# Kernel tuning notes

Measured on AMD Instinct MI355X. Metric: run time of the kernel, lower is better.

The kernel has to match this reference:

```python
import jax, jax.numpy as jnp
import numpy as np

N = 100000
E = 1600000
F_IN, F_HID, F_OUT = 512, 512, 256
NEG_SLOPE = 0.01  # nn.LeakyReLU default


def setup_inputs() -> dict:
    key = jax.random.key(0)
    ks = jax.random.split(key, 16)
    def lin(k, fi, fo):
        s = 1.0 / np.sqrt(fi)
        return jax.random.uniform(k, (fi, fo), jnp.float32, -s, s)
    inp = {
        'x': jax.random.normal(ks[0], (N, F_IN), jnp.float32),
        'edge_index': jax.random.randint(ks[1], (2, E), 0, N, jnp.int64),
        'W1': lin(ks[2], F_IN, F_HID), 'b1': jnp.zeros((F_HID,), jnp.float32),
        'W2': lin(ks[3], F_HID, F_HID), 'b2': jnp.zeros((F_HID,), jnp.float32),
        'W3': lin(ks[4], F_HID, F_HID), 'b3': jnp.zeros((F_HID,), jnp.float32),
        'W4': lin(ks[5], F_HID, F_OUT), 'b4': jnp.zeros((F_OUT,), jnp.float32),
        'fcW1': lin(ks[6], F_OUT, 64), 'fcb1': jnp.zeros((64,), jnp.float32),
        'fcW2': lin(ks[7], 64, 1), 'fcb2': jnp.zeros((1,), jnp.float32),
    }
    return inp


def _gcn_norm(edge_index):
    # PyG gcn_norm with add_self_loops=True: deg counts incoming edges + 1 self loop
    src, dst = edge_index[0], edge_index[1]
    deg = jax.ops.segment_sum(jnp.ones((E,), jnp.float32), dst, num_segments=N) + 1.0
    dis = jax.lax.rsqrt(deg)  # deg >= 1 always (self loops)
    edge_norm = dis[src] * dis[dst]  # [E]
    self_norm = dis * dis            # [N], norm for the added self loop
    return src, dst, edge_norm, self_norm


def _gcn_layer(x, src, dst, edge_norm, self_norm, W, b):
    xw = x @ W  # transform-then-propagate (in < out not an issue here)
    agg = jax.ops.segment_sum(xw[src] * edge_norm[:, None], dst, num_segments=N)
    return agg + self_norm[:, None] * xw + b


def leaky(x):
    return jnp.where(x >= 0, x, NEG_SLOPE * x)


def reference(x, edge_index, W1, b1, W2, b2, W3, b3, W4, b4, fcW1, fcb1, fcW2, fcb2):
    src, dst, en, sn = _gcn_norm(edge_index)
    h = leaky(_gcn_layer(x, src, dst, en, sn, W1, b1))
    h = leaky(_gcn_layer(h, src, dst, en, sn, W2, b2))
    h = leaky(_gcn_layer(h, src, dst, en, sn, W3, b3))
    h = leaky(_gcn_layer(h, src, dst, en, sn, W4, b4))
    g = jnp.mean(h, axis=0, keepdims=True)  # global_mean_pool, batch=None -> [1, F_OUT]
    g = leaky(g @ fcW1 + fcb1)
    # dropout is identity in eval mode
    g = g @ fcW2 + fcb2
    return jax.nn.sigmoid(g)  # [1, 1]
```

## Files before the change

kernel.cpp:

```cpp
#include <hip/hip_runtime.h>
#include <hip/hip_bf16.h>
#include <cstdint>
#include <cstddef>


typedef unsigned short u16;
typedef unsigned char u8;
typedef unsigned int u32;
typedef u16 u16x4 __attribute__((ext_vector_type(4)));
typedef u16 u16x8 __attribute__((ext_vector_type(8)));
typedef u32 u32x2 __attribute__((ext_vector_type(2)));
typedef float f32x2 __attribute__((ext_vector_type(2)));
typedef float f32x4 __attribute__((ext_vector_type(4)));

__device__ __forceinline__ u16 f2bf(float f) {
  u32 u = __builtin_bit_cast(u32, f);
  u += 0x7fffu + ((u >> 16) & 1u);
  return (u16)(u >> 16);
}
__device__ __forceinline__ float bf2f(u16 h) {
  return __builtin_bit_cast(float, (u32)h << 16);
}
__device__ __forceinline__ void g2lds16(const void* g, void* l) {
  __builtin_amdgcn_global_load_lds((__attribute__((address_space(1))) void*)g,
                                   (__attribute__((address_space(3))) void*)l, 16, 0, 0);
}

__global__ __launch_bounds__(256) void init_kernel(int* __restrict__ deg,
                                                   int* __restrict__ cursor,
                                                   float* __restrict__ pool, int N) {
  int i = blockIdx.x * 256 + threadIdx.x;
  if (i < N) { deg[i] = 0; cursor[i] = 0; }
  if (i < 256) pool[i] = 0.f;
}

__global__ void detect_kernel(const int* __restrict__ ei, int* __restrict__ flag) {
  __shared__ int nz;
  if (threadIdx.x == 0) nz = 0;
  __syncthreads();
  if (ei[2 * threadIdx.x + 1] != 0) atomicAdd(&nz, 1);
  __syncthreads();
  if (threadIdx.x == 0) *flag = (nz == 0) ? 1 : 0;
}

__device__ __forceinline__ int ld_src(const int* ei, int E, int e, int f64) {
  return f64 ? (int)((const long long*)ei)[e] : ei[e];
}
__device__ __forceinline__ int ld_dst(const int* ei, int E, int e, int f64) {
  return f64 ? (int)((const long long*)ei)[(long long)E + e] : ei[E + e];
}

__global__ __launch_bounds__(256) void degree_kernel(const int* __restrict__ ei,
                                                     const int* __restrict__ flag,
                                                     int* __restrict__ deg, int E) {
  int e = blockIdx.x * 256 + threadIdx.x;
  if (e >= E) return;
  int f = *flag;
  atomicAdd(&deg[ld_dst(ei, E, e, f)], 1);
}

__global__ __launch_bounds__(256) void dis_kernel(const int* __restrict__ deg,
                                                  float* __restrict__ dis, int N) {
  int i = blockIdx.x * 256 + threadIdx.x;
  if (i < N) dis[i] = rsqrtf((float)deg[i] + 1.0f);
}

__global__ __launch_bounds__(1024) void scan1_kernel(const int* __restrict__ deg,
                                                     int* __restrict__ rs,
                                                     int* __restrict__ bsum, int N) {
  __shared__ int s[1024];
  int tid = threadIdx.x;
  int i = blockIdx.x * 1024 + tid;
  int v = (i < N) ? deg[i] : 0;
  s[tid] = v;
  __syncthreads();
  for (int off = 1; off < 1024; off <<= 1) {
    int t = (tid >= off) ? s[tid - off] : 0;
    __syncthreads();
    s[tid] += t;
    __syncthreads();
  }
  if (i < N) rs[i] = s[tid] - v;
  if (tid == 1023) bsum[blockIdx.x] = s[1023];
}

__global__ __launch_bounds__(1024) void scan2_kernel(const int* __restrict__ bsum,
                                                     int* __restrict__ boff, int nb) {
  __shared__ int s[1024];
  int tid = threadIdx.x;
  int v = (tid < nb) ? bsum[tid] : 0;
  s[tid] = v;
  __syncthreads();
  for (int off = 1; off < 1024; off <<= 1) {
    int t = (tid >= off) ? s[tid - off] : 0;
    __syncthreads();
    s[tid] += t;
    __syncthreads();
  }
  if (tid < nb) boff[tid] = s[tid] - v;
}

__global__ __launch_bounds__(256) void scan3_kernel(int* __restrict__ rs,
                                                    const int* __restrict__ boff, int N) {
  int i = blockIdx.x * 256 + threadIdx.x;
  if (i < N) rs[i] += boff[i >> 10];
}

__global__ __launch_bounds__(256) void fill_kernel(const int* __restrict__ ei,
                                                   const int* __restrict__ flag,
                                                   const int* __restrict__ rs,
                                                   int* __restrict__ cursor,
                                                   int* __restrict__ colv, int E) {
  int e = blockIdx.x * 256 + threadIdx.x;
  if (e >= E) return;
  int f = *flag;
  int s = ld_src(ei, E, e, f);
  int d = ld_dst(ei, E, e, f);
  int p = atomicAdd(&cursor[d], 1);
  colv[rs[d] + p] = s;
}

__global__ __launch_bounds__(256) void convx_kernel(const float* __restrict__ x,
                                                    u8* __restrict__ x8, size_t n) {
  size_t i = ((size_t)blockIdx.x * 256 + threadIdx.x) * 4;
  if (i >= n) return;
  float4 v = *reinterpret_cast<const float4*>(x + i);
  int lo = __builtin_amdgcn_cvt_pk_fp8_f32(v.x, v.y, 0, false);
  int r = __builtin_amdgcn_cvt_pk_fp8_f32(v.z, v.w, lo, true);
  size_t row = i >> 9;
  int col = (int)(i & 511);
  int sw = ((int)(row & 7)) << 3;
  *reinterpret_cast<u32*>(x8 + row * 512 + (col ^ sw)) = (u32)r;
}

__global__ __launch_bounds__(256) void convw_kernel(const float* __restrict__ W,
                                                    u8* __restrict__ Wt, int Nout) {
  int id = blockIdx.x * 256 + threadIdx.x;
  if (id >= 512 * Nout) return;
  int k = id / Nout, nn = id - k * Nout;
  float v = W[id];
  int e = __builtin_amdgcn_cvt_pk_fp8_f32(v, v, 0, false);
  Wt[nn * 512 + (k ^ ((nn & 7) << 3))] = (u8)e;
}

__global__ __launch_bounds__(256, 2)
void gemm8_kernel(const u8* __restrict__ A, const u8* __restrict__ Bt,
                  u8* __restrict__ Cout, int M, int Nout) {
  __shared__ u8 sA[128 * 64];
  __shared__ u8 sB[128 * 64];
  const int tid = threadIdx.x;
  const int wave = tid >> 6, lane = tid & 63;
  const int m0 = blockIdx.x * 128;
  const int n0 = blockIdx.y * 128;
  const int wm = (wave >> 1) * 64, wn = (wave & 1) * 64;
  const int srow = tid >> 2;
  const int soff = (tid & 3) * 16;
  const int fr = lane & 15, fq8 = (lane >> 4) * 8;
  const int xa = (fr & 7) << 3;

  f32x4 acc[4][4];
#pragma unroll
  for (int i = 0; i < 4; ++i)
#pragma unroll
    for (int j = 0; j < 4; ++j) acc[i][j] = (f32x4){0.f, 0.f, 0.f, 0.f};

  int ar0 = m0 + srow;      if (ar0 >= M) ar0 = M - 1;
  int ar1 = m0 + 64 + srow; if (ar1 >= M) ar1 = M - 1;
  const size_t a0 = (size_t)ar0 * 512 + soff;
  const size_t a1 = (size_t)ar1 * 512 + soff;
  const size_t b0 = (size_t)(n0 + srow) * 512 + soff;
  const size_t b1 = (size_t)(n0 + 64 + srow) * 512 + soff;

  for (int k0 = 0; k0 < 512; k0 += 64) {
    g2lds16(A + a0 + k0, &sA[wave * 1024]);
    g2lds16(A + a1 + k0, &sA[4096 + wave * 1024]);
    g2lds16(Bt + b0 + k0, &sB[wave * 1024]);
    g2lds16(Bt + b1 + k0, &sB[4096 + wave * 1024]);
    __builtin_amdgcn_s_waitcnt(0);
    __syncthreads();

    long long af[2][4], bf[2][4];
#pragma unroll
    for (int t = 0; t < 4; ++t) {
      const int ra = (wm + t * 16 + fr) * 64;
      const int rb = (wn + t * 16 + fr) * 64;
#pragma unroll
      for (int s = 0; s < 2; ++s) {
        af[s][t] = *reinterpret_cast<const long long*>(&sA[ra + ((s * 32 + fq8) ^ xa)]);
        bf[s][t] = *reinterpret_cast<const long long*>(&sB[rb + ((s * 32 + fq8) ^ xa)]);
      }
    }
#pragma unroll
    for (int i = 0; i < 4; ++i)
#pragma unroll
      for (int j = 0; j < 4; ++j) {
        acc[i][j] = __builtin_amdgcn_mfma_f32_16x16x32_fp8_fp8(af[0][i], bf[0][j], acc[i][j], 0, 0, 0);
        acc[i][j] = __builtin_amdgcn_mfma_f32_16x16x32_fp8_fp8(af[1][i], bf[1][j], acc[i][j], 0, 0, 0);
      }
    __syncthreads();
  }

  const int crow0 = m0 + wm + ((lane >> 4) << 2);
  const int ccol0 = n0 + wn + (lane & 15);
#pragma unroll
  for (int j = 0; j < 4; ++j) {
    const int col = ccol0 + j * 16;
#pragma unroll
    for (int i = 0; i < 4; ++i)
#pragma unroll
      for (int r = 0; r < 4; ++r) {
        int row = crow0 + i * 16 + r;
        if (row < M) {
          float v = acc[i][j][r];
          int e = __builtin_amdgcn_cvt_pk_fp8_f32(v, v, 0, false);
          Cout[(size_t)row * Nout + (col ^ ((row & 7) << 3))] = (u8)e;
        }
      }
  }
}

__global__ __launch_bounds__(256)
void agg_kernel(const u8* __restrict__ xw, const int* __restrict__ colv,
                const int* __restrict__ rs, const int* __restrict__ deg,
                const float* __restrict__ dis, const float* __restrict__ bias,
                u8* __restrict__ hout, int N) {
  const int wave = threadIdx.x >> 6;
  const int lane = threadIdx.x & 63;
  const int node = blockIdx.x * 4 + wave;
  if (node >= N) return;
  const int start = rs[node];
  const int d = deg[node];
  const float dd = dis[node];
  const int fo = lane * 8;

  f32x2 acc[4];
#pragma unroll
  for (int i = 0; i < 4; ++i) acc[i] = (f32x2){0.f, 0.f};

  const int total = d + 1;
  for (int base = 0; base < total; base += 64) {
    int t = base + lane;
    int s = node;
    float w = 0.f;
    if (t < d)       { s = colv[start + t]; w = dd * dis[s]; }
    else if (t == d) { w = dd * dd; }
    int cnt = total - base;
    if (cnt > 64) cnt = 64;
    int cnt8 = (cnt + 7) & ~7;
    int wi = __builtin_bit_cast(int, w);
    for (int j = 0; j < cnt8; j += 8) {
      u32x2 v[8];
      float ws[8];
#pragma unroll
      for (int k = 0; k < 8; ++k) {
        int sk = __builtin_amdgcn_readlane(s, j + k);
        ws[k] = __builtin_bit_cast(float, __builtin_amdgcn_readlane(wi, j + k));
        v[k] = *reinterpret_cast<const u32x2*>(xw + (size_t)sk * 512 + (fo ^ ((sk & 7) << 3)));
      }
#pragma unroll
      for (int k = 0; k < 8; ++k) {
        f32x2 p0 = __builtin_amdgcn_cvt_pk_f32_fp8((int)v[k].x, false);
        f32x2 p1 = __builtin_amdgcn_cvt_pk_f32_fp8((int)v[k].x, true);
        f32x2 p2 = __builtin_amdgcn_cvt_pk_f32_fp8((int)v[k].y, false);
        f32x2 p3 = __builtin_amdgcn_cvt_pk_f32_fp8((int)v[k].y, true);
        f32x2 wv = (f32x2){ws[k], ws[k]};
        acc[0] += wv * p0;
        acc[1] += wv * p1;
        acc[2] += wv * p2;
        acc[3] += wv * p3;
      }
    }
  }

  float h[8];
#pragma unroll
  for (int i = 0; i < 8; ++i) {
    float v = (i & 1) ? acc[i >> 1].y : acc[i >> 1].x;
    v += bias[fo + i];
    v = v >= 0.f ? v : 0.01f * v;
    h[i] = v;
  }
  int lo = __builtin_amdgcn_cvt_pk_fp8_f32(h[0], h[1], 0, false);
  lo = __builtin_amdgcn_cvt_pk_fp8_f32(h[2], h[3], lo, true);
  int hi = __builtin_amdgcn_cvt_pk_fp8_f32(h[4], h[5], 0, false);
  hi = __builtin_amdgcn_cvt_pk_fp8_f32(h[6], h[7], hi, true);
  u32x2 o; o.x = (u32)lo; o.y = (u32)hi;
  __builtin_nontemporal_store(o, reinterpret_cast<u32x2*>(
      hout + (size_t)node * 512 + (fo ^ ((node & 7) << 3))));
}

__global__ __launch_bounds__(256)
void agg256_kernel(const u8* __restrict__ xw, const int* __restrict__ colv,
                   const int* __restrict__ rs, const int* __restrict__ deg,
                   const float* __restrict__ dis, const float* __restrict__ bias,
                   u16* __restrict__ hout, int N) {
  const int wave = threadIdx.x >> 6;
  const int lane = threadIdx.x & 63;
  const int node = blockIdx.x * 4 + wave;
  if (node >= N) return;
  const int start = rs[node];
  const int d = deg[node];
  const float dd = dis[node];
  const int fo = lane * 4;

  f32x2 acc[2];
  acc[0] = (f32x2){0.f, 0.f};
  acc[1] = (f32x2){0.f, 0.f};

  const int total = d + 1;
  for (int base = 0; base < total; base += 64) {
    int t = base + lane;
    int s = node;
    float w = 0.f;
    if (t < d)       { s = colv[start + t]; w = dd * dis[s]; }
    else if (t == d) { w = dd * dd; }
    int cnt = total - base;
    if (cnt > 64) cnt = 64;
    int cnt8 = (cnt + 7) & ~7;
    int wi = __builtin_bit_cast(int, w);
    for (int j = 0; j < cnt8; j += 8) {
      u32 v[8];
      float ws[8];
#pragma unroll
      for (int k = 0; k < 8; ++k) {
        int sk = __builtin_amdgcn_readlane(s, j + k);
        ws[k] = __builtin_bit_cast(float, __builtin_amdgcn_readlane(wi, j + k));
        v[k] = *reinterpret_cast<const u32*>(xw + (size_t)sk * 256 + (fo ^ ((sk & 7) << 3)));
      }
#pragma unroll
      for (int k = 0; k < 8; ++k) {
        f32x2 p0 = __builtin_amdgcn_cvt_pk_f32_fp8((int)v[k], false);
        f32x2 p1 = __builtin_amdgcn_cvt_pk_f32_fp8((int)v[k], true);
        f32x2 wv = (f32x2){ws[k], ws[k]};
        acc[0] += wv * p0;
        acc[1] += wv * p1;
      }
    }
  }

  u16x4 o;
#pragma unroll
  for (int i = 0; i < 4; ++i) {
    float v = (i & 1) ? acc[i >> 1].y : acc[i >> 1].x;
    v += bias[fo + i];
    v = v >= 0.f ? v : 0.01f * v;
    o[i] = f2bf(v);
  }
  *reinterpret_cast<u16x4*>(hout + (size_t)node * 256 + fo) = o;
}

__global__ __launch_bounds__(256) void pool_kernel(const u16* __restrict__ h,
                                                   float* __restrict__ pool, int N) {
  __shared__ float lds[8 * 256];
  const int tid = threadIdx.x;
  const int fg = tid & 31;
  const int rg = tid >> 5;
  float acc[8];
#pragma unroll
  for (int i = 0; i < 8; ++i) acc[i] = 0.f;
  for (int r = blockIdx.x * 8 + rg; r < N; r += gridDim.x * 8) {
    u16x8 v = *reinterpret_cast<const u16x8*>(h + (size_t)r * 256 + fg * 8);
#pragma unroll
    for (int i = 0; i < 8; ++i) acc[i] += bf2f(v[i]);
  }
#pragma unroll
  for (int i = 0; i < 8; ++i) lds[rg * 256 + fg * 8 + i] = acc[i];
  __syncthreads();
  float s = 0.f;
#pragma unroll
  for (int g = 0; g < 8; ++g) s += lds[g * 256 + tid];
  atomicAdd(&pool[tid], s);
}

__global__ void fc_kernel(const float* __restrict__ pool, const float* __restrict__ fcW1,
                          const float* __restrict__ fcb1, const float* __restrict__ fcW2,
                          const float* __restrict__ fcb2, float* __restrict__ out,
                          float invN) {
  int j = threadIdx.x;
  float acc = 0.f;
  for (int f = 0; f < 256; ++f) acc += pool[f] * invN * fcW1[f * 64 + j];
  float h = acc + fcb1[j];
  h = h >= 0.f ? h : 0.01f * h;
  float p = h * fcW2[j];
  for (int o = 32; o; o >>= 1) p += __shfl_down(p, o);
  if (j == 0) out[0] = 1.f / (1.f + expf(-(p + fcb2[0])));
}

extern "C" void kernel_launch(void* const* d_in, const int* in_sizes, int n_in,
                              void* d_out, int out_size, void* d_ws, size_t ws_size,
                              hipStream_t stream) {
  const float* x    = (const float*)d_in[0];
  const int*   ei   = (const int*)d_in[1];
  const float* W1   = (const float*)d_in[2];
  const float* b1   = (const float*)d_in[3];
  const float* W2   = (const float*)d_in[4];
  const float* b2   = (const float*)d_in[5];
  const float* W3   = (const float*)d_in[6];
  const float* b3   = (const float*)d_in[7];
  const float* W4   = (const float*)d_in[8];
  const float* b4   = (const float*)d_in[9];
  const float* fcW1 = (const float*)d_in[10];
  const float* fcb1 = (const float*)d_in[11];
  const float* fcW2 = (const float*)d_in[12];
  const float* fcb2 = (const float*)d_in[13];
  float* out = (float*)d_out;

  const int N = in_sizes[0] / 512;
  const int E = in_sizes[1] / 2;

  char* p = (char*)d_ws;
  auto carve = [&](size_t bytes) {
    char* r = p;
    p += (bytes + 255) & ~(size_t)255;
    return r;
  };
  u8*  bufX = (u8*)carve((size_t)N * 512);
  u8*  bufP = (u8*)carve((size_t)N * 512);
  u8*  bufQ = (u8*)carve((size_t)N * 512);
  u16* bufH4 = (u16*)carve((size_t)N * 256 * 2);
  u8* Wt1 = (u8*)carve(512 * 512);
  u8* Wt2 = (u8*)carve(512 * 512);
  u8* Wt3 = (u8*)carve(512 * 512);
  u8* Wt4 = (u8*)carve(512 * 256);
  int* deg    = (int*)carve((size_t)N * 4);
  int* cursor = (int*)carve((size_t)N * 4);
  int* rs     = (int*)carve((size_t)(N + 1) * 4);
  int* colv   = (int*)carve((size_t)E * 4);
  int* bsum   = (int*)carve(1024 * 4);
  int* boff   = (int*)carve(1024 * 4);
  int* flag   = (int*)carve(256);
  float* disv = (float*)carve((size_t)N * 4);
  float* pool = (float*)carve(256 * 4);
  if ((size_t)(p - (char*)d_ws) > ws_size) return;

  const int nb1024 = (N + 1023) / 1024;

  init_kernel<<<(N + 255) / 256, 256, 0, stream>>>(deg, cursor, pool, N);
  detect_kernel<<<1, 256, 0, stream>>>(ei, flag);
  degree_kernel<<<(E + 255) / 256, 256, 0, stream>>>(ei, flag, deg, E);
  dis_kernel<<<(N + 255) / 256, 256, 0, stream>>>(deg, disv, N);
  scan1_kernel<<<nb1024, 1024, 0, stream>>>(deg, rs, bsum, N);
  scan2_kernel<<<1, 1024, 0, stream>>>(bsum, boff, nb1024);
  scan3_kernel<<<(N + 255) / 256, 256, 0, stream>>>(rs, boff, N);
  fill_kernel<<<(E + 255) / 256, 256, 0, stream>>>(ei, flag, rs, cursor, colv, E);

  convx_kernel<<<((size_t)N * 512 / 4 + 255) / 256, 256, 0, stream>>>(x, bufX, (size_t)N * 512);
  convw_kernel<<<(512 * 512 + 255) / 256, 256, 0, stream>>>(W1, Wt1, 512);
  convw_kernel<<<(512 * 512 + 255) / 256, 256, 0, stream>>>(W2, Wt2, 512);
  convw_kernel<<<(512 * 512 + 255) / 256, 256, 0, stream>>>(W3, Wt3, 512);
  convw_kernel<<<(512 * 256 + 255) / 256, 256, 0, stream>>>(W4, Wt4, 256);

  const unsigned gm = (unsigned)((N + 127) / 128);
  const unsigned ga = (unsigned)((N + 3) / 4);

  gemm8_kernel<<<dim3(gm, 4), 256, 0, stream>>>(bufX, Wt1, bufP, N, 512);
  agg_kernel<<<ga, 256, 0, stream>>>(bufP, colv, rs, deg, disv, b1, bufQ, N);
  gemm8_kernel<<<dim3(gm, 4), 256, 0, stream>>>(bufQ, Wt2, bufP, N, 512);
  agg_kernel<<<ga, 256, 0, stream>>>(bufP, colv, rs, deg, disv, b2, bufX, N);
  gemm8_kernel<<<dim3(gm, 4), 256, 0, stream>>>(bufX, Wt3, bufP, N, 512);
  agg_kernel<<<ga, 256, 0, stream>>>(bufP, colv, rs, deg, disv, b3, bufQ, N);
  gemm8_kernel<<<dim3(gm, 2), 256, 0, stream>>>(bufQ, Wt4, bufP, N, 256);
  agg256_kernel<<<ga, 256, 0, stream>>>(bufP, colv, rs, deg, disv, b4, bufH4, N);

  pool_kernel<<<256, 256, 0, stream>>>(bufH4, pool, N);
  fc_kernel<<<1, 64, 0, stream>>>(pool, fcW1, fcb1, fcW2, fcb2, out, 1.0f / (float)N);
}
```

Measured before the change: 1.137 ms.

## Precompute edge weights in CSR, widen gather loads, and remap GEMM blocks per XCD

The CSR fill now stores each edge's source together with its normalization weight, so the aggregation kernels no longer do a dependent dis[s] gather. Aggregation lanes are split into two halves that each handle a different edge and load 16 (or 8) contiguous bytes, with the halves combined by a cross-half shuffle at the end. The GEMM output swizzle is dropped so gathers read contiguous rows, and the GEMM grid is flattened with a block-index remap that keeps M-tiles sharing an A tile on the same XCD. The costs are a doubled edge-array footprint and an extra shuffle reduction per node.

```diff
diff --git a/kernel.cpp b/kernel.cpp
--- a/kernel.cpp
+++ b/kernel.cpp
@@ -10,6 +10,7 @@
 typedef u16 u16x4 __attribute__((ext_vector_type(4)));
 typedef u16 u16x8 __attribute__((ext_vector_type(8)));
 typedef u32 u32x2 __attribute__((ext_vector_type(2)));
+typedef u32 u32x4 __attribute__((ext_vector_type(4)));
 typedef float f32x2 __attribute__((ext_vector_type(2)));
 typedef float f32x4 __attribute__((ext_vector_type(4)));
 
@@ -110,14 +111,19 @@
                                                    const int* __restrict__ flag,
                                                    const int* __restrict__ rs,
                                                    int* __restrict__ cursor,
-                                                   int* __restrict__ colv, int E) {
+                                                   const float* __restrict__ dis,
+                                                   u32x2* __restrict__ ev, int E) {
   int e = blockIdx.x * 256 + threadIdx.x;
   if (e >= E) return;
   int f = *flag;
   int s = ld_src(ei, E, e, f);
   int d = ld_dst(ei, E, e, f);
   int p = atomicAdd(&cursor[d], 1);
-  colv[rs[d] + p] = s;
+  float w = dis[s] * dis[d];
+  u32x2 t;
+  t.x = (u32)s;
+  t.y = __builtin_bit_cast(u32, w);
+  ev[rs[d] + p] = t;
 }
 
 __global__ __launch_bounds__(256) void convx_kernel(const float* __restrict__ x,
@@ -145,13 +151,19 @@
 
 __global__ __launch_bounds__(256, 2)
 void gemm8_kernel(const u8* __restrict__ A, const u8* __restrict__ Bt,
-                  u8* __restrict__ Cout, int M, int Nout) {
+                  u8* __restrict__ Cout, int M, int Nout, int gm, int lgy) {
+  const int id = blockIdx.x;
+  const int xcd = id & 7, q = id >> 3;
+  const int by = q & ((1 << lgy) - 1);
+  const int bx = ((q >> lgy) << 3) + xcd;
+  if (bx >= gm) return;
+
   __shared__ u8 sA[128 * 64];
   __shared__ u8 sB[128 * 64];
   const int tid = threadIdx.x;
   const int wave = tid >> 6, lane = tid & 63;
-  const int m0 = blockIdx.x * 128;
-  const int n0 = blockIdx.y * 128;
+  const int m0 = bx * 128;
+  const int n0 = by * 128;
   const int wm = (wave >> 1) * 64, wn = (wave & 1) * 64;
   const int srow = tid >> 2;
   const int soff = (tid & 3) * 16;
@@ -213,14 +225,14 @@
         if (row < M) {
           float v = acc[i][j][r];
           int e = __builtin_amdgcn_cvt_pk_fp8_f32(v, v, 0, false);
-          Cout[(size_t)row * Nout + (col ^ ((row & 7) << 3))] = (u8)e;
+          Cout[(size_t)row * Nout + col] = (u8)e;
         }
       }
   }
 }
 
 __global__ __launch_bounds__(256)
-void agg_kernel(const u8* __restrict__ xw, const int* __restrict__ colv,
+void agg_kernel(const u8* __restrict__ xw, const u32x2* __restrict__ ev,
                 const int* __restrict__ rs, const int* __restrict__ deg,
                 const float* __restrict__ dis, const float* __restrict__ bias,
                 u8* __restrict__ hout, int N) {
@@ -231,52 +243,63 @@
   const int start = rs[node];
   const int d = deg[node];
   const float dd = dis[node];
-  const int fo = lane * 8;
-
-  f32x2 acc[4];
-#pragma unroll
-  for (int i = 0; i < 4; ++i) acc[i] = (f32x2){0.f, 0.f};
+  const int half = lane >> 5;
+  const int col = lane & 31;
+
+  f32x2 acc[8];
+#pragma unroll
+  for (int i = 0; i < 8; ++i) acc[i] = (f32x2){0.f, 0.f};
 
   const int total = d + 1;
   for (int base = 0; base < total; base += 64) {
     int t = base + lane;
     int s = node;
     float w = 0.f;
-    if (t < d)       { s = colv[start + t]; w = dd * dis[s]; }
+    if (t < d)       { u32x2 e = ev[start + t]; s = (int)e.x; w = __builtin_bit_cast(float, e.y); }
     else if (t == d) { w = dd * dd; }
     int cnt = total - base;
     if (cnt > 64) cnt = 64;
     int cnt8 = (cnt + 7) & ~7;
     int wi = __builtin_bit_cast(int, w);
     for (int j = 0; j < cnt8; j += 8) {
-      u32x2 v[8];
-      float ws[8];
-#pragma unroll
-      for (int k = 0; k < 8; ++k) {
-        int sk = __builtin_amdgcn_readlane(s, j + k);
-        ws[k] = __builtin_bit_cast(float, __builtin_amdgcn_readlane(wi, j + k));
-        v[k] = *reinterpret_cast<const u32x2*>(xw + (size_t)sk * 512 + (fo ^ ((sk & 7) << 3)));
-      }
-#pragma unroll
-      for (int k = 0; k < 8; ++k) {
-        f32x2 p0 = __builtin_amdgcn_cvt_pk_f32_fp8((int)v[k].x, false);
-        f32x2 p1 = __builtin_amdgcn_cvt_pk_f32_fp8((int)v[k].x, true);
-        f32x2 p2 = __builtin_amdgcn_cvt_pk_f32_fp8((int)v[k].y, false);
-        f32x2 p3 = __builtin_amdgcn_cvt_pk_f32_fp8((int)v[k].y, true);
-        f32x2 wv = (f32x2){ws[k], ws[k]};
-        acc[0] += wv * p0;
-        acc[1] += wv * p1;
-        acc[2] += wv * p2;
-        acc[3] += wv * p3;
+      u32x4 v[4];
+      float wp[4];
+#pragma unroll
+      for (int p = 0; p < 4; ++p) {
+        int s0 = __builtin_amdgcn_readlane(s, j + 2 * p);
+        int s1 = __builtin_amdgcn_readlane(s, j + 2 * p + 1);
+        int w0 = __builtin_amdgcn_readlane(wi, j + 2 * p);
+        int w1 = __builtin_amdgcn_readlane(wi, j + 2 * p + 1);
+        int sm = half ? s1 : s0;
+        wp[p] = __builtin_bit_cast(float, half ? w1 : w0);
+        v[p] = *reinterpret_cast<const u32x4*>(xw + (size_t)sm * 512 + col * 16);
+      }
+#pragma unroll
+      for (int p = 0; p < 4; ++p) {
+        f32x2 wv = (f32x2){wp[p], wp[p]};
+#pragma unroll
+        for (int qq = 0; qq < 4; ++qq) {
+          f32x2 lo = __builtin_amdgcn_cvt_pk_f32_fp8((int)v[p][qq], false);
+          f32x2 hi = __builtin_amdgcn_cvt_pk_f32_fp8((int)v[p][qq], true);
+          acc[2 * qq]     += wv * lo;
+          acc[2 * qq + 1] += wv * hi;
+        }
       }
     }
   }
 
+#pragma unroll
+  for (int i = 0; i < 8; ++i) {
+    acc[i].x += __shfl_xor(acc[i].x, 32);
+    acc[i].y += __shfl_xor(acc[i].y, 32);
+  }
+
+  const int f0 = col * 16 + half * 8;
   float h[8];
 #pragma unroll
   for (int i = 0; i < 8; ++i) {
-    float v = (i & 1) ? acc[i >> 1].y : acc[i >> 1].x;
-    v += bias[fo + i];
+    float v = (i & 1) ? acc[half * 4 + (i >> 1)].y : acc[half * 4 + (i >> 1)].x;
+    v += bias[f0 + i];
     v = v >= 0.f ? v : 0.01f * v;
     h[i] = v;
   }
@@ -286,11 +309,11 @@
   hi = __builtin_amdgcn_cvt_pk_fp8_f32(h[6], h[7], hi, true);
   u32x2 o; o.x = (u32)lo; o.y = (u32)hi;
   __builtin_nontemporal_store(o, reinterpret_cast<u32x2*>(
-      hout + (size_t)node * 512 + (fo ^ ((node & 7) << 3))));
+      hout + (size_t)node * 512 + (f0 ^ ((node & 7) << 3))));
 }
 
 __global__ __launch_bounds__(256)
-void agg256_kernel(const u8* __restrict__ xw, const int* __restrict__ colv,
+void agg256_kernel(const u8* __restrict__ xw, const u32x2* __restrict__ ev,
                    const int* __restrict__ rs, const int* __restrict__ deg,
                    const float* __restrict__ dis, const float* __restrict__ bias,
                    u16* __restrict__ hout, int N) {
@@ -301,52 +324,68 @@
   const int start = rs[node];
   const int d = deg[node];
   const float dd = dis[node];
-  const int fo = lane * 4;
-
-  f32x2 acc[2];
-  acc[0] = (f32x2){0.f, 0.f};
-  acc[1] = (f32x2){0.f, 0.f};
+  const int half = lane >> 5;
+  const int col = lane & 31;
+
+  f32x2 acc[4];
+#pragma unroll
+  for (int i = 0; i < 4; ++i) acc[i] = (f32x2){0.f, 0.f};
 
   const int total = d + 1;
   for (int base = 0; base < total; base += 64) {
     int t = base + lane;
     int s = node;
     float w = 0.f;
-    if (t < d)       { s = colv[start + t]; w = dd * dis[s]; }
+    if (t < d)       { u32x2 e = ev[start + t]; s = (int)e.x; w = __builtin_bit_cast(float, e.y); }
     else if (t == d) { w = dd * dd; }
     int cnt = total - base;
     if (cnt > 64) cnt = 64;
     int cnt8 = (cnt + 7) & ~7;
     int wi = __builtin_bit_cast(int, w);
     for (int j = 0; j < cnt8; j += 8) {
-      u32 v[8];
-      float ws[8];
-#pragma unroll
-      for (int k = 0; k < 8; ++k) {
-        int sk = __builtin_amdgcn_readlane(s, j + k);
-        ws[k] = __builtin_bit_cast(float, __builtin_amdgcn_readlane(wi, j + k));
-        v[k] = *reinterpret_cast<const u32*>(xw + (size_t)sk * 256 + (fo ^ ((sk & 7) << 3)));
-      }
-#pragma unroll
-      for (int k = 0; k < 8; ++k) {
-        f32x2 p0 = __builtin_amdgcn_cvt_pk_f32_fp8((int)v[k], false);
-        f32x2 p1 = __builtin_amdgcn_cvt_pk_f32_fp8((int)v[k], true);
-        f32x2 wv = (f32x2){ws[k], ws[k]};
+      u32x2 v[4];
+      float wp[4];
+#pragma unroll
+      for (int p = 0; p < 4; ++p) {
+        int s0 = __builtin_amdgcn_readlane(s, j + 2 * p);
+        int s1 = __builtin_amdgcn_readlane(s, j + 2 * p + 1);
+        int w0 = __builtin_amdgcn_readlane(wi, j + 2 * p);
+        int w1 = __builtin_amdgcn_readlane(wi, j + 2 * p + 1);
+        int sm = half ? s1 : s0;
+        wp[p] = __builtin_bit_cast(float, half ? w1 : w0);
+        v[p] = *reinterpret_cast<const u32x2*>(xw + (size_t)sm * 256 + col * 8);
+      }
+#pragma unroll
+      for (int p = 0; p < 4; ++p) {
+        f32x2 wv = (f32x2){wp[p], wp[p]};
+        f32x2 p0 = __builtin_amdgcn_cvt_pk_f32_fp8((int)v[p].x, false);
+        f32x2 p1 = __builtin_amdgcn_cvt_pk_f32_fp8((int)v[p].x, true);
+        f32x2 p2 = __builtin_amdgcn_cvt_pk_f32_fp8((int)v[p].y, false);
+        f32x2 p3 = __builtin_amdgcn_cvt_pk_f32_fp8((int)v[p].y, true);
         acc[0] += wv * p0;
         acc[1] += wv * p1;
+        acc[2] += wv * p2;
+        acc[3] += wv * p3;
       }
     }
   }
 
+#pragma unroll
+  for (int i = 0; i < 4; ++i) {
+    acc[i].x += __shfl_xor(acc[i].x, 32);
+    acc[i].y += __shfl_xor(acc[i].y, 32);
+  }
+
+  const int f0 = col * 8 + half * 4;
   u16x4 o;
 #pragma unroll
   for (int i = 0; i < 4; ++i) {
-    float v = (i & 1) ? acc[i >> 1].y : acc[i >> 1].x;
-    v += bias[fo + i];
+    float v = (i & 1) ? acc[half * 2 + (i >> 1)].y : acc[half * 2 + (i >> 1)].x;
+    v += bias[f0 + i];
     v = v >= 0.f ? v : 0.01f * v;
     o[i] = f2bf(v);
   }
-  *reinterpret_cast<u16x4*>(hout + (size_t)node * 256 + fo) = o;
+  *reinterpret_cast<u16x4*>(hout + (size_t)node * 256 + f0) = o;
 }
 
 __global__ __launch_bounds__(256) void pool_kernel(const u16* __restrict__ h,
@@ -425,7 +464,7 @@
   int* deg    = (int*)carve((size_t)N * 4);
   int* cursor = (int*)carve((size_t)N * 4);
   int* rs     = (int*)carve((size_t)(N + 1) * 4);
-  int* colv   = (int*)carve((size_t)E * 4);
+  u32x2* ev   = (u32x2*)carve((size_t)E * 8);
   int* bsum   = (int*)carve(1024 * 4);
   int* boff   = (int*)carve(1024 * 4);
   int* flag   = (int*)carve(256);
@@ -442,7 +481,7 @@
   scan1_kernel<<<nb1024, 1024, 0, stream>>>(deg, rs, bsum, N);
   scan2_kernel<<<1, 1024, 0, stream>>>(bsum, boff, nb1024);
   scan3_kernel<<<(N + 255) / 256, 256, 0, stream>>>(rs, boff, N);
-  fill_kernel<<<(E + 255) / 256, 256, 0, stream>>>(ei, flag, rs, cursor, colv, E);
+  fill_kernel<<<(E + 255) / 256, 256, 0, stream>>>(ei, flag, rs, cursor, disv, ev, E);
 
   convx_kernel<<<((size_t)N * 512 / 4 + 255) / 256, 256, 0, stream>>>(x, bufX, (size_t)N * 512);
   convw_kernel<<<(512 * 512 + 255) / 256, 256, 0, stream>>>(W1, Wt1, 512);
@@ -450,17 +489,18 @@
   convw_kernel<<<(512 * 512 + 255) / 256, 256, 0, stream>>>(W3, Wt3, 512);
   convw_kernel<<<(512 * 256 + 255) / 256, 256, 0, stream>>>(W4, Wt4, 256);
 
-  const unsigned gm = (unsigned)((N + 127) / 128);
+  const int gm = (N + 127) / 128;
+  const int gm8 = (gm + 7) & ~7;
   const unsigned ga = (unsigned)((N + 3) / 4);
 
-  gemm8_kernel<<<dim3(gm, 4), 256, 0, stream>>>(bufX, Wt1, bufP, N, 512);
-  agg_kernel<<<ga, 256, 0, stream>>>(bufP, colv, rs, deg, disv, b1, bufQ, N);
-  gemm8_kernel<<<dim3(gm, 4), 256, 0, stream>>>(bufQ, Wt2, bufP, N, 512);
-  agg_kernel<<<ga, 256, 0, stream>>>(bufP, colv, rs, deg, disv, b2, bufX, N);
-  gemm8_kernel<<<dim3(gm, 4), 256, 0, stream>>>(bufX, Wt3, bufP, N, 512);
-  agg_kernel<<<ga, 256, 0, stream>>>(bufP, colv, rs, deg, disv, b3, bufQ, N);
-  gemm8_kernel<<<dim3(gm, 2), 256, 0, stream>>>(bufQ, Wt4, bufP, N, 256);
-  agg256_kernel<<<ga, 256, 0, stream>>>(bufP, colv, rs, deg, disv, b4, bufH4, N);
+  gemm8_kernel<<<gm8 * 4, 256, 0, stream>>>(bufX, Wt1, bufP, N, 512, gm, 2);
+  agg_kernel<<<ga, 256, 0, stream>>>(bufP, ev, rs, deg, disv, b1, bufQ, N);
+  gemm8_kernel<<<gm8 * 4, 256, 0, stream>>>(bufQ, Wt2, bufP, N, 512, gm, 2);
+  agg_kernel<<<ga, 256, 0, stream>>>(bufP, ev, rs, deg, disv, b2, bufX, N);
+  gemm8_kernel<<<gm8 * 4, 256, 0, stream>>>(bufX, Wt3, bufP, N, 512, gm, 2);
+  agg_kernel<<<ga, 256, 0, stream>>>(bufP, ev, rs, deg, disv, b3, bufQ, N);
+  gemm8_kernel<<<gm8 * 2, 256, 0, stream>>>(bufQ, Wt4, bufP, N, 256, gm, 1);
+  agg256_kernel<<<ga, 256, 0, stream>>>(bufP, ev, rs, deg, disv, b4, bufH4, N);
 
   pool_kernel<<<256, 256, 0, stream>>>(bufH4, pool, N);
   fc_kernel<<<1, 64, 0, stream>>>(pool, fcW1, fcb1, fcW2, fcb2, out, 1.0f / (float)N);
```

Result: no change. 1.149 ms (+1.0%).

## Precompute edge weights in CSR, drop swizzle on GEMM output, XCD-aware GEMM grid

Applied to the files above, without the earlier changes.

The CSR fill now stores each edge as a (source, normalized weight) pair, so aggregation kernels avoid a dependent random gather of dis[src]. GEMM outputs are written in plain row layout and the gathers read them without the XOR swizzle. The GEMM grid is flattened and remapped so consecutive row tiles share an XCD, aiming for better L2 reuse of the weight tiles. The edge array doubles in size, adding bandwidth on the edge-stream reads.

```diff
diff --git a/kernel.cpp b/kernel.cpp
--- a/kernel.cpp
+++ b/kernel.cpp
@@ -110,14 +110,19 @@
                                                    const int* __restrict__ flag,
                                                    const int* __restrict__ rs,
                                                    int* __restrict__ cursor,
-                                                   int* __restrict__ colv, int E) {
+                                                   const float* __restrict__ dis,
+                                                   u32x2* __restrict__ ev, int E) {
   int e = blockIdx.x * 256 + threadIdx.x;
   if (e >= E) return;
   int f = *flag;
   int s = ld_src(ei, E, e, f);
   int d = ld_dst(ei, E, e, f);
   int p = atomicAdd(&cursor[d], 1);
-  colv[rs[d] + p] = s;
+  float w = dis[s] * dis[d];
+  u32x2 t;
+  t.x = (u32)s;
+  t.y = __builtin_bit_cast(u32, w);
+  ev[rs[d] + p] = t;
 }
 
 __global__ __launch_bounds__(256) void convx_kernel(const float* __restrict__ x,
@@ -145,13 +150,19 @@
 
 __global__ __launch_bounds__(256, 2)
 void gemm8_kernel(const u8* __restrict__ A, const u8* __restrict__ Bt,
-                  u8* __restrict__ Cout, int M, int Nout) {
+                  u8* __restrict__ Cout, int M, int Nout, int gm, int lgy) {
+  const int id = blockIdx.x;
+  const int xcd = id & 7, q = id >> 3;
+  const int by = q & ((1 << lgy) - 1);
+  const int bx = ((q >> lgy) << 3) + xcd;
+  if (bx >= gm) return;
+
   __shared__ u8 sA[128 * 64];
   __shared__ u8 sB[128 * 64];
   const int tid = threadIdx.x;
   const int wave = tid >> 6, lane = tid & 63;
-  const int m0 = blockIdx.x * 128;
-  const int n0 = blockIdx.y * 128;
+  const int m0 = bx * 128;
+  const int n0 = by * 128;
   const int wm = (wave >> 1) * 64, wn = (wave & 1) * 64;
   const int srow = tid >> 2;
   const int soff = (tid & 3) * 16;
@@ -213,14 +224,14 @@
         if (row < M) {
           float v = acc[i][j][r];
           int e = __builtin_amdgcn_cvt_pk_fp8_f32(v, v, 0, false);
-          Cout[(size_t)row * Nout + (col ^ ((row & 7) << 3))] = (u8)e;
+          Cout[(size_t)row * Nout + col] = (u8)e;
         }
       }
   }
 }
 
 __global__ __launch_bounds__(256)
-void agg_kernel(const u8* __restrict__ xw, const int* __restrict__ colv,
+void agg_kernel(const u8* __restrict__ xw, const u32x2* __restrict__ ev,
                 const int* __restrict__ rs, const int* __restrict__ deg,
                 const float* __restrict__ dis, const float* __restrict__ bias,
                 u8* __restrict__ hout, int N) {
@@ -242,7 +253,7 @@
     int t = base + lane;
     int s = node;
     float w = 0.f;
-    if (t < d)       { s = colv[start + t]; w = dd * dis[s]; }
+    if (t < d)       { u32x2 e = ev[start + t]; s = (int)e.x; w = __builtin_bit_cast(float, e.y); }
     else if (t == d) { w = dd * dd; }
     int cnt = total - base;
     if (cnt > 64) cnt = 64;
@@ -255,7 +266,7 @@
       for (int k = 0; k < 8; ++k) {
         int sk = __builtin_amdgcn_readlane(s, j + k);
         ws[k] = __builtin_bit_cast(float, __builtin_amdgcn_readlane(wi, j + k));
-        v[k] = *reinterpret_cast<const u32x2*>(xw + (size_t)sk * 512 + (fo ^ ((sk & 7) << 3)));
+        v[k] = *reinterpret_cast<const u32x2*>(xw + (size_t)sk * 512 + fo);
       }
 #pragma unroll
       for (int k = 0; k < 8; ++k) {
@@ -290,7 +301,7 @@
 }
 
 __global__ __launch_bounds__(256)
-void agg256_kernel(const u8* __restrict__ xw, const int* __restrict__ colv,
+void agg256_kernel(const u8* __restrict__ xw, const u32x2* __restrict__ ev,
                    const int* __restrict__ rs, const int* __restrict__ deg,
                    const float* __restrict__ dis, const float* __restrict__ bias,
                    u16* __restrict__ hout, int N) {
@@ -312,7 +323,7 @@
     int t = base + lane;
     int s = node;
     float w = 0.f;
-    if (t < d)       { s = colv[start + t]; w = dd * dis[s]; }
+    if (t < d)       { u32x2 e = ev[start + t]; s = (int)e.x; w = __builtin_bit_cast(float, e.y); }
     else if (t == d) { w = dd * dd; }
     int cnt = total - base;
     if (cnt > 64) cnt = 64;
@@ -325,7 +336,7 @@
       for (int k = 0; k < 8; ++k) {
         int sk = __builtin_amdgcn_readlane(s, j + k);
         ws[k] = __builtin_bit_cast(float, __builtin_amdgcn_readlane(wi, j + k));
-        v[k] = *reinterpret_cast<const u32*>(xw + (size_t)sk * 256 + (fo ^ ((sk & 7) << 3)));
+        v[k] = *reinterpret_cast<const u32*>(xw + (size_t)sk * 256 + fo);
       }
 #pragma unroll
       for (int k = 0; k < 8; ++k) {
@@ -425,7 +436,7 @@
   int* deg    = (int*)carve((size_t)N * 4);
   int* cursor = (int*)carve((size_t)N * 4);
   int* rs     = (int*)carve((size_t)(N + 1) * 4);
-  int* colv   = (int*)carve((size_t)E * 4);
+  u32x2* ev   = (u32x2*)carve((size_t)E * 8);
   int* bsum   = (int*)carve(1024 * 4);
   int* boff   = (int*)carve(1024 * 4);
   int* flag   = (int*)carve(256);
@@ -442,7 +453,7 @@
   scan1_kernel<<<nb1024, 1024, 0, stream>>>(deg, rs, bsum, N);
   scan2_kernel<<<1, 1024, 0, stream>>>(bsum, boff, nb1024);
   scan3_kernel<<<(N + 255) / 256, 256, 0, stream>>>(rs, boff, N);
-  fill_kernel<<<(E + 255) / 256, 256, 0, stream>>>(ei, flag, rs, cursor, colv, E);
+  fill_kernel<<<(E + 255) / 256, 256, 0, stream>>>(ei, flag, rs, cursor, disv, ev, E);
 
   convx_kernel<<<((size_t)N * 512 / 4 + 255) / 256, 256, 0, stream>>>(x, bufX, (size_t)N * 512);
   convw_kernel<<<(512 * 512 + 255) / 256, 256, 0, stream>>>(W1, Wt1, 512);
@@ -450,17 +461,18 @@
   convw_kernel<<<(512 * 512 + 255) / 256, 256, 0, stream>>>(W3, Wt3, 512);
   convw_kernel<<<(512 * 256 + 255) / 256, 256, 0, stream>>>(W4, Wt4, 256);
 
-  const unsigned gm = (unsigned)((N + 127) / 128);
+  const int gm = (N + 127) / 128;
+  const int gm8 = (gm + 7) & ~7;
   const unsigned ga = (unsigned)((N + 3) / 4);
 
-  gemm8_kernel<<<dim3(gm, 4), 256, 0, stream>>>(bufX, Wt1, bufP, N, 512);
-  agg_kernel<<<ga, 256, 0, stream>>>(bufP, colv, rs, deg, disv, b1, bufQ, N);
-  gemm8_kernel<<<dim3(gm, 4), 256, 0, stream>>>(bufQ, Wt2, bufP, N, 512);
-  agg_kernel<<<ga, 256, 0, stream>>>(bufP, colv, rs, deg, disv, b2, bufX, N);
-  gemm8_kernel<<<dim3(gm, 4), 256, 0, stream>>>(bufX, Wt3, bufP, N, 512);
-  agg_kernel<<<ga, 256, 0, stream>>>(bufP, colv, rs, deg, disv, b3, bufQ, N);
-  gemm8_kernel<<<dim3(gm, 2), 256, 0, stream>>>(bufQ, Wt4, bufP, N, 256);
-  agg256_kernel<<<ga, 256, 0, stream>>>(bufP, colv, rs, deg, disv, b4, bufH4, N);
+  gemm8_kernel<<<gm8 * 4, 256, 0, stream>>>(bufX, Wt1, bufP, N, 512, gm, 2);
+  agg_kernel<<<ga, 256, 0, stream>>>(bufP, ev, rs, deg, disv, b1, bufQ, N);
+  gemm8_kernel<<<gm8 * 4, 256, 0, stream>>>(bufQ, Wt2, bufP, N, 512, gm, 2);
+  agg_kernel<<<ga, 256, 0, stream>>>(bufP, ev, rs, deg, disv, b2, bufX, N);
+  gemm8_kernel<<<gm8 * 4, 256, 0, stream>>>(bufX, Wt3, bufP, N, 512, gm, 2);
+  agg_kernel<<<ga, 256, 0, stream>>>(bufP, ev, rs, deg, disv, b3, bufQ, N);
+  gemm8_kernel<<<gm8 * 2, 256, 0, stream>>>(bufQ, Wt4, bufP, N, 256, gm, 1);
+  agg256_kernel<<<ga, 256, 0, stream>>>(bufP, ev, rs, deg, disv, b4, bufH4, N);
 
   pool_kernel<<<256, 256, 0, stream>>>(bufH4, pool, N);
   fc_kernel<<<1, 64, 0, stream>>>(pool, fcW1, fcb1, fcW2, fcb2, out, 1.0f / (float)N);
```

New measurement: 1.103 ms. 3.0% less time.
